# Optimization experiments

Measured on AMD Instinct MI355X. Metric: run time of the kernel, lower is better.

Reference implementation:

```python
import jax, jax.numpy as jnp
import numpy as np

EPS = 1e-5
NH, NP = 4, 4  # num_heads, num_points (num_levels = 1)


def layer_norm(x, g, b):
    m = jnp.mean(x, -1, keepdims=True)
    xc = x - m
    v = jnp.mean(xc * xc, -1, keepdims=True)
    return xc * jax.lax.rsqrt(v + EPS) * g + b


def setup_inputs() -> dict:
    key = jax.random.key(0)
    ks = jax.random.split(key, 8)
    B, C, H, W = 8, 256, 64, 64
    s = 0.02
    return {
        "x1": jax.random.normal(ks[0], (B, C, H, W), jnp.float32),
        "x2": jax.random.normal(ks[1], (B, C, H, W), jnp.float32),
        "ln1_g": jnp.ones((C,), jnp.float32),
        "ln1_b": jnp.zeros((C,), jnp.float32),
        "ln2_g": jnp.ones((C,), jnp.float32),
        "ln2_b": jnp.zeros((C,), jnp.float32),
        "pos_scale": jnp.ones((1,), jnp.float32),
        "W_off": jax.random.normal(ks[2], (C, NH * NP * 2), jnp.float32) * s,
        "b_off": jax.random.normal(ks[3], (NH * NP * 2,), jnp.float32) * 0.5,
        "W_att": jax.random.normal(ks[4], (C, NH * NP), jnp.float32) * s,
        "b_att": jnp.zeros((NH * NP,), jnp.float32),
        "W_val": jax.random.normal(ks[5], (C, C), jnp.float32) * s,
        "b_val": jnp.zeros((C,), jnp.float32),
        "W_out": jax.random.normal(ks[6], (C, C), jnp.float32) * s,
        "b_out": jnp.zeros((C,), jnp.float32),
    }


def reference(x1, x2, ln1_g, ln1_b, ln2_g, ln2_b, pos_scale,
              W_off, b_off, W_att, b_att, W_val, b_val, W_out, b_out):
    B, C, H, W = x1.shape
    Nq = H * W
    d = C // NH
    q_in = x1.reshape(B, C, Nq).transpose(0, 2, 1)   # (B, Nq, C)
    v_in = x2.reshape(B, C, Nq).transpose(0, 2, 1)   # (B, Nv, C), identity

    # ScaledSinuEmbedding positional encoding over the query sequence
    inv_freq = 1.0 / (10000.0 ** (jnp.arange(0, C, 2, dtype=jnp.float32) / C))
    sinu = jnp.arange(Nq, dtype=jnp.float32)[:, None] * inv_freq[None, :]
    qpos = jnp.concatenate([jnp.sin(sinu), jnp.cos(sinu)], -1) * pos_scale  # (Nq, C)

    query = layer_norm(q_in, ln1_g, ln1_b) + qpos[None]
    value = layer_norm(v_in, ln2_g, ln2_b) @ W_val + b_val                 # (B, Nv, C)
    value = value.reshape(B, Nq, NH, d).transpose(0, 2, 1, 3)              # (B, NH, Nv, d)

    off = (query @ W_off + b_off).reshape(B, Nq, NH, NP, 2)
    att = jax.nn.softmax((query @ W_att + b_att).reshape(B, Nq, NH, NP), axis=-1)

    # reference points: normalized pixel centers of the query grid
    ry, rx = jnp.meshgrid((jnp.arange(H, dtype=jnp.float32) + 0.5) / H,
                          (jnp.arange(W, dtype=jnp.float32) + 0.5) / W,
                          indexing="ij")
    ref = jnp.stack([rx.ravel(), ry.ravel()], -1)                          # (Nq, 2) as (x, y)

    norm = jnp.array([W, H], jnp.float32)  # offset_normalizer = (W, H)
    loc = ref[None, :, None, None, :] + off / norm                         # (B,Nq,NH,NP,2)
    loc = loc.transpose(0, 2, 1, 3, 4)                                     # (B,NH,Nq,NP,2)
    # grid_sample(align_corners=False): pixel = normalized * size - 0.5
    px = loc[..., 0] * W - 0.5
    py = loc[..., 1] * H - 0.5
    x0 = jnp.floor(px); y0 = jnp.floor(py)
    wx = px - x0; wy = py - y0
    x0i = x0.astype(jnp.int32); y0i = y0.astype(jnp.int32)

    def gather(ix, iy):
        # zero padding for out-of-bounds corners, like grid_sample(padding_mode='zeros')
        valid = ((ix >= 0) & (ix < W) & (iy >= 0) & (iy < H)).astype(value.dtype)
        idx = jnp.clip(iy, 0, H - 1) * W + jnp.clip(ix, 0, W - 1)          # (B,NH,Nq,NP)
        g = jnp.take_along_axis(value, idx.reshape(B, NH, Nq * NP, 1), axis=2)
        return g.reshape(B, NH, Nq, NP, d) * valid[..., None]

    sampled = (gather(x0i, y0i) * ((1 - wx) * (1 - wy))[..., None]
               + gather(x0i + 1, y0i) * (wx * (1 - wy))[..., None]
               + gather(x0i, y0i + 1) * ((1 - wx) * wy)[..., None]
               + gather(x0i + 1, y0i + 1) * (wx * wy)[..., None])          # (B,NH,Nq,NP,d)

    out = jnp.sum(sampled * att.transpose(0, 2, 1, 3)[..., None], axis=3)  # (B,NH,Nq,d)
    out = out.transpose(0, 2, 1, 3).reshape(B, Nq, C)
    out = out @ W_out + b_out + v_in                                       # + identity (x2)
    return out.transpose(0, 2, 1).reshape(B, C, H, W)
```

## Files before the change

### kernel.cpp

```cpp
#include <hip/hip_runtime.h>
#include <math.h>

namespace {
constexpr int kC = 256;
constexpr int kNq = 4096;
constexpr int kM = 32768;
}

typedef __attribute__((ext_vector_type(8))) short short8;
typedef __attribute__((ext_vector_type(4))) float f32x4;

__device__ inline unsigned short f2bf(float f) {
  union { float f; unsigned u; } v; v.f = f;
  unsigned r = (v.u + 0x7FFFu + ((v.u >> 16) & 1u)) >> 16;
  return (unsigned short)r;
}
__device__ inline float uasf(unsigned u) {
  union { unsigned u; float f; } v; v.u = u; return v.f;
}

__global__ __launch_bounds__(256)
void prep_weights_kernel(const float* __restrict__ Wv, const float* __restrict__ Wo,
                         const float* __restrict__ Woff, const float* __restrict__ Watt,
                         unsigned short* __restrict__ WvT, unsigned short* __restrict__ WoT,
                         unsigned short* __restrict__ WoaT) {
  const int i = blockIdx.x * 256 + threadIdx.x;
  {
    const int n = i >> 8, k = i & 255;
    WvT[i] = f2bf(Wv[k * 256 + n]);
    WoT[i] = f2bf(Wo[k * 256 + n]);
  }
  if (i < 16384) {
    const int j = i >> 8, k = i & 255;
    float v = 0.f;
    if (j < 32) v = Woff[k * 32 + j];
    else if (j < 48) v = Watt[k * 16 + (j - 32)];
    WoaT[i] = f2bf(v);
  }
}

__global__ __launch_bounds__(256)
void fused_ln_gemm_kernel(const float* __restrict__ x1, const float* __restrict__ x2,
                          const float* __restrict__ ln1_g, const float* __restrict__ ln1_b,
                          const float* __restrict__ ln2_g, const float* __restrict__ ln2_b,
                          const float* __restrict__ ps,
                          const unsigned short* __restrict__ WvT,
                          const float* __restrict__ b_val, unsigned short* __restrict__ V,
                          const unsigned short* __restrict__ WoaT,
                          const float* __restrict__ boff, const float* __restrict__ batt,
                          float* __restrict__ RAW) {
  __shared__ unsigned short As[64][264];
  __shared__ float scratch[256][33];
  __shared__ float psum[8][32];
  __shared__ float psq[8][32];
  __shared__ float smean[64];
  __shared__ float srstd[64];

  const int mode = blockIdx.x & 1;
  const int m0 = (blockIdx.x >> 1) * 64;
  const int b = m0 >> 12;
  const int n0 = m0 & 4095;
  const int tid = threadIdx.x;
  const float* X = mode ? x1 : x2;
  const float gc = mode ? ln1_g[tid] : ln2_g[tid];
  const float bc = mode ? ln1_b[tid] : ln2_b[tid];
  float scale = 0.f, invf = 0.f;
  if (mode) {
    scale = ps[0];
    const int i2 = (tid < 128) ? tid : (tid - 128);
    invf = powf(10000.f, -(float)(2 * i2) * (1.f / 256.f));
  }
  const float* Xb = X + (size_t)b * kC * kNq;

  for (int grp = 0; grp < 2; ++grp) {
    float4 vbuf[8];
#pragma unroll
    for (int it = 0; it < 8; ++it) {
      const int i = it * 256 + tid;
      const int c = i >> 3, q4 = (i & 7) * 4;
      vbuf[it] = *(const float4*)&Xb[(size_t)c * kNq + n0 + grp * 32 + q4];
    }
#pragma unroll
    for (int it = 0; it < 8; ++it) {
      const int i = it * 256 + tid;
      const int c = i >> 3, q4 = (i & 7) * 4;
      scratch[c][q4 + 0] = vbuf[it].x;
      scratch[c][q4 + 1] = vbuf[it].y;
      scratch[c][q4 + 2] = vbuf[it].z;
      scratch[c][q4 + 3] = vbuf[it].w;
    }
    __syncthreads();
    {
      const int nn = tid & 31, cg = tid >> 5;
      float s = 0.f, sq = 0.f;
#pragma unroll
      for (int cc = 0; cc < 32; ++cc) {
        const float v = scratch[cg * 32 + cc][nn];
        s += v; sq += v * v;
      }
      psum[cg][nn] = s; psq[cg][nn] = sq;
    }
    __syncthreads();
    if (tid < 32) {
      float S = 0.f, Q = 0.f;
#pragma unroll
      for (int g = 0; g < 8; ++g) { S += psum[g][tid]; Q += psq[g][tid]; }
      const float m = S * (1.f / 256.f);
      const float v = Q * (1.f / 256.f) - m * m;
      smean[grp * 32 + tid] = m;
      srstd[grp * 32 + tid] = rsqrtf(v + 1e-5f);
    }
    __syncthreads();
    if (mode) {
      for (int q = 0; q < 32; ++q) {
        const int row = grp * 32 + q;
        float val = (scratch[tid][q] - smean[row]) * srstd[row] * gc + bc;
        const float a = (float)(n0 + row) * invf;
        val += ((tid < 128) ? sinf(a) : cosf(a)) * scale;
        As[row][tid] = f2bf(val);
      }
    } else {
      for (int q = 0; q < 32; ++q) {
        const int row = grp * 32 + q;
        As[row][tid] = f2bf((scratch[tid][q] - smean[row]) * srstd[row] * gc + bc);
      }
    }
    __syncthreads();
  }

  const int lane = tid & 63, w = tid >> 6;
  const int l15 = lane & 15, quad = lane >> 4;

  if (mode == 0) {
    f32x4 acc[4][4];
#pragma unroll
    for (int i = 0; i < 4; ++i)
#pragma unroll
      for (int j = 0; j < 4; ++j) acc[i][j] = (f32x4){0.f, 0.f, 0.f, 0.f};
#pragma unroll
    for (int s = 0; s < 8; ++s) {
      short8 af[4], wf[4];
#pragma unroll
      for (int t = 0; t < 4; ++t) af[t] = *(const short8*)&As[t * 16 + l15][s * 32 + quad * 8];
#pragma unroll
      for (int t = 0; t < 4; ++t)
        wf[t] = *(const short8*)&WvT[(size_t)(w * 64 + t * 16 + l15) * 256 + s * 32 + quad * 8];
#pragma unroll
      for (int i = 0; i < 4; ++i)
#pragma unroll
        for (int j = 0; j < 4; ++j)
          acc[i][j] = __builtin_amdgcn_mfma_f32_16x16x32_bf16(af[i], wf[j], acc[i][j], 0, 0, 0);
    }
#pragma unroll
    for (int i = 0; i < 4; ++i)
#pragma unroll
      for (int j = 0; j < 4; ++j) {
        const int n = w * 64 + j * 16 + l15;
        const float bn = b_val[n];
#pragma unroll
        for (int r = 0; r < 4; ++r) {
          const int m = m0 + i * 16 + quad * 4 + r;
          V[(size_t)m * 256 + n] = f2bf(acc[i][j][r] + bn);
        }
      }
  } else {
    f32x4 acc[3];
#pragma unroll
    for (int j = 0; j < 3; ++j) acc[j] = (f32x4){0.f, 0.f, 0.f, 0.f};
#pragma unroll
    for (int s = 0; s < 8; ++s) {
      short8 af = *(const short8*)&As[w * 16 + l15][s * 32 + quad * 8];
      short8 wf[3];
#pragma unroll
      for (int t = 0; t < 3; ++t)
        wf[t] = *(const short8*)&WoaT[(size_t)(t * 16 + l15) * 256 + s * 32 + quad * 8];
#pragma unroll
      for (int j = 0; j < 3; ++j)
        acc[j] = __builtin_amdgcn_mfma_f32_16x16x32_bf16(af, wf[j], acc[j], 0, 0, 0);
    }
#pragma unroll
    for (int j = 0; j < 3; ++j) {
      const int n = j * 16 + l15;
      const float bn = (n < 32) ? boff[n] : batt[n - 32];
#pragma unroll
      for (int r = 0; r < 4; ++r) {
        const int m = m0 + w * 16 + quad * 4 + r;
        RAW[(size_t)m * 48 + n] = acc[j][r] + bn;
      }
    }
  }
}

__global__ __launch_bounds__(256)
void sample_out_kernel(const float* __restrict__ RAW, const unsigned short* __restrict__ V,
                       const unsigned short* __restrict__ Wt,
                       const float* __restrict__ bias, const float* __restrict__ x2,
                       float* __restrict__ OUT) {
  __shared__ unsigned short Bs[64][264];
  __shared__ __align__(16) char smemA[32768];
  int (*sidx)[4] = (int(*)[4])smemA;
  float (*swgt)[4] = (float(*)[4])(smemA + 16384);
  float* ot = (float*)smemA;

  const int blk = blockIdx.x;
  const int b = blk & 7;
  const int tile = blk >> 3;
  const int m0 = b * 4096 + tile * 64;
  const int tid = threadIdx.x;

#pragma unroll
  for (int t = 0; t < 4; ++t) {
    const int trip = t * 256 + tid;
    const int q_l = trip >> 4, h = (trip >> 2) & 3, p = trip & 3;
    const int m = m0 + q_l;
    const float* raw = RAW + (size_t)m * 48;
    const float l0 = raw[32 + h * 4 + 0];
    const float l1 = raw[32 + h * 4 + 1];
    const float l2 = raw[32 + h * 4 + 2];
    const float l3 = raw[32 + h * 4 + 3];
    const float mx = fmaxf(fmaxf(l0, l1), fmaxf(l2, l3));
    const float e0 = expf(l0 - mx), e1 = expf(l1 - mx), e2 = expf(l2 - mx), e3 = expf(l3 - mx);
    const float lp = (p == 0) ? e0 : (p == 1) ? e1 : (p == 2) ? e2 : e3;
    const float attp = lp / (e0 + e1 + e2 + e3);

    const float ox = raw[h * 8 + p * 2 + 0];
    const float oy = raw[h * 8 + p * 2 + 1];
    const float px = (float)(m & 63) + ox;
    const float py = (float)((m >> 6) & 63) + oy;
    const float fx = floorf(px), fy = floorf(py);
    const float wx = px - fx, wy = py - fy;
    const int x0 = (int)fx, y0 = (int)fy;
#pragma unroll
    for (int c = 0; c < 4; ++c) {
      const int dx = c & 1, dy = c >> 1;
      const int xx = x0 + dx, yy = y0 + dy;
      const bool valid = (xx >= 0) & (xx < 64) & (yy >= 0) & (yy < 64);
      const float wc = (dx ? wx : 1.f - wx) * (dy ? wy : 1.f - wy) * attp;
      swgt[trip][c] = valid ? wc : 0.f;
      const int xc = min(max(xx, 0), 63), yc = min(max(yy, 0), 63);
      sidx[trip][c] = yc * 64 + xc;
    }
  }
  __syncthreads();

#pragma unroll
  for (int it = 0; it < 8; ++it) {
    const int lin = it * 256 + tid;
    const int q_l = lin >> 5, sub = lin & 31;
    const int h = sub >> 3, c8 = (sub & 7) * 8;
    const int trip0 = q_l * 16 + h * 4;
    const unsigned short* vb = V + (size_t)b * kNq * kC + h * 64 + c8;
    float acc[8] = {};
#pragma unroll
    for (int p = 0; p < 4; ++p) {
      const int4 idx = *(const int4*)&sidx[trip0 + p][0];
      const float4 wv = *(const float4*)&swgt[trip0 + p][0];
      const int ia[4] = {idx.x, idx.y, idx.z, idx.w};
      const float wa[4] = {wv.x, wv.y, wv.z, wv.w};
#pragma unroll
      for (int c = 0; c < 4; ++c) {
        const uint4 u = *(const uint4*)&vb[(size_t)ia[c] * kC];
        const float w = wa[c];
        acc[0] = fmaf(w, uasf(u.x << 16), acc[0]);
        acc[1] = fmaf(w, uasf(u.x & 0xffff0000u), acc[1]);
        acc[2] = fmaf(w, uasf(u.y << 16), acc[2]);
        acc[3] = fmaf(w, uasf(u.y & 0xffff0000u), acc[3]);
        acc[4] = fmaf(w, uasf(u.z << 16), acc[4]);
        acc[5] = fmaf(w, uasf(u.z & 0xffff0000u), acc[5]);
        acc[6] = fmaf(w, uasf(u.w << 16), acc[6]);
        acc[7] = fmaf(w, uasf(u.w & 0xffff0000u), acc[7]);
      }
    }
    short8 outv;
#pragma unroll
    for (int e = 0; e < 8; ++e) outv[e] = (short)f2bf(acc[e]);
    *(short8*)&Bs[q_l][h * 64 + c8] = outv;
  }
  __syncthreads();

  const int lane = tid & 63, w = tid >> 6;
  const int l15 = lane & 15, quad = lane >> 4;
  f32x4 acc[4][4];
#pragma unroll
  for (int i = 0; i < 4; ++i)
#pragma unroll
    for (int j = 0; j < 4; ++j) acc[i][j] = (f32x4){0.f, 0.f, 0.f, 0.f};
#pragma unroll
  for (int s = 0; s < 8; ++s) {
    short8 wf[4], bf[4];
#pragma unroll
    for (int t = 0; t < 4; ++t)
      wf[t] = *(const short8*)&Wt[(size_t)(w * 64 + t * 16 + l15) * 256 + s * 32 + quad * 8];
#pragma unroll
    for (int t = 0; t < 4; ++t) bf[t] = *(const short8*)&Bs[t * 16 + l15][s * 32 + quad * 8];
#pragma unroll
    for (int i = 0; i < 4; ++i)
#pragma unroll
      for (int j = 0; j < 4; ++j)
        acc[i][j] = __builtin_amdgcn_mfma_f32_16x16x32_bf16(wf[i], bf[j], acc[i][j], 0, 0, 0);
  }

  const int whalf = w >> 1;
  const int clbase = (w & 1) * 64;
  for (int ch = 0; ch < 2; ++ch) {
    __syncthreads();
    if (whalf == ch) {
#pragma unroll
      for (int i = 0; i < 4; ++i)
#pragma unroll
        for (int j = 0; j < 4; ++j)
#pragma unroll
          for (int r = 0; r < 4; ++r)
            ot[(clbase + i * 16 + quad * 4 + r) * 64 + j * 16 + l15] = acc[i][j][r];
    }
    __syncthreads();
#pragma unroll
    for (int t = 0; t < 8; ++t) {
      const int lin = t * 256 + tid;
      const int cl = lin >> 4, q4 = (lin & 15) * 4;
      const int c = ch * 128 + cl;
      const size_t rowbase = ((size_t)b * 256 + c) * 4096 + tile * 64;
      const float4 xv = *(const float4*)&x2[rowbase + q4];
      const float bc = bias[c];
      float4 o;
      o.x = ot[cl * 64 + q4 + 0] + bc + xv.x;
      o.y = ot[cl * 64 + q4 + 1] + bc + xv.y;
      o.z = ot[cl * 64 + q4 + 2] + bc + xv.z;
      o.w = ot[cl * 64 + q4 + 3] + bc + xv.w;
      *(float4*)&OUT[rowbase + q4] = o;
    }
  }
}

extern "C" void kernel_launch(void* const* d_in, const int* in_sizes, int n_in,
                              void* d_out, int out_size, void* d_ws, size_t ws_size,
                              hipStream_t stream) {
  const float* x1 = (const float*)d_in[0];
  const float* x2 = (const float*)d_in[1];
  const float* ln1_g = (const float*)d_in[2];
  const float* ln1_b = (const float*)d_in[3];
  const float* ln2_g = (const float*)d_in[4];
  const float* ln2_b = (const float*)d_in[5];
  const float* pos_scale = (const float*)d_in[6];
  const float* W_off = (const float*)d_in[7];
  const float* b_off = (const float*)d_in[8];
  const float* W_att = (const float*)d_in[9];
  const float* b_att = (const float*)d_in[10];
  const float* W_val = (const float*)d_in[11];
  const float* b_val = (const float*)d_in[12];
  const float* W_out = (const float*)d_in[13];
  const float* b_out = (const float*)d_in[14];
  float* out = (float*)d_out;

  char* ws = (char*)d_ws;
  const size_t plane2 = (size_t)kM * kC * sizeof(unsigned short);
  unsigned short* Vb   = (unsigned short*)(ws);
  float* RAW           = (float*)(ws + plane2);
  unsigned short* WvT  = (unsigned short*)(ws + plane2 + (size_t)kM * 48 * 4);
  unsigned short* WoT  = WvT + 65536;
  unsigned short* WoaT = WoT + 65536;

  prep_weights_kernel<<<256, 256, 0, stream>>>(W_val, W_out, W_off, W_att, WvT, WoT, WoaT);
  fused_ln_gemm_kernel<<<1024, 256, 0, stream>>>(x1, x2, ln1_g, ln1_b, ln2_g, ln2_b,
                                                 pos_scale, WvT, b_val, Vb,
                                                 WoaT, b_off, b_att, RAW);
  sample_out_kernel<<<512, 256, 0, stream>>>(RAW, Vb, WoT, b_out, x2, out);
}
```

Before: 185.0 us.

## Precompute positional-encoding projection once; restructure LN stats with register loads and shuffles

Uses linearity to split the offset/attention projection: the positional-encoding term times W_off/W_att plus bias is computed once per query position in the weight-prep kernel (QP) and added in the epilogue. This removes per-element sin/cos from the per-batch LN kernel. The LayerNorm path now loads all input tiles into registers up front, reduces sums with wave shuffles, and stages x in LDS as bf16 instead of fp32. That shrinks LDS use but normalizes from bf16-rounded inputs, which adds precision error.

```diff
diff --git a/kernel.cpp b/kernel.cpp
--- a/kernel.cpp
+++ b/kernel.cpp
@@ -8,6 +8,7 @@
 }
 
 typedef __attribute__((ext_vector_type(8))) short short8;
+typedef __attribute__((ext_vector_type(4))) short short4v;
 typedef __attribute__((ext_vector_type(4))) float f32x4;
 
 __device__ inline unsigned short f2bf(float f) {
@@ -15,6 +16,9 @@
   unsigned r = (v.u + 0x7FFFu + ((v.u >> 16) & 1u)) >> 16;
   return (unsigned short)r;
 }
+__device__ inline float bf2f(unsigned short h) {
+  union { unsigned u; float f; } v; v.u = ((unsigned)h) << 16; return v.f;
+}
 __device__ inline float uasf(unsigned u) {
   union { unsigned u; float f; } v; v.u = u; return v.f;
 }
@@ -22,9 +26,14 @@
 __global__ __launch_bounds__(256)
 void prep_weights_kernel(const float* __restrict__ Wv, const float* __restrict__ Wo,
                          const float* __restrict__ Woff, const float* __restrict__ Watt,
+                         const float* __restrict__ boff, const float* __restrict__ batt,
+                         const float* __restrict__ ps,
                          unsigned short* __restrict__ WvT, unsigned short* __restrict__ WoT,
-                         unsigned short* __restrict__ WoaT) {
-  const int i = blockIdx.x * 256 + threadIdx.x;
+                         unsigned short* __restrict__ WoaT, float* __restrict__ QP) {
+  __shared__ unsigned short Aq[64][264];
+  const int blk = blockIdx.x;
+  const int tid = threadIdx.x;
+  const int i = blk * 256 + tid;
   {
     const int n = i >> 8, k = i & 255;
     WvT[i] = f2bf(Wv[k * 256 + n]);
@@ -37,22 +46,61 @@
     else if (j < 48) v = Watt[k * 16 + (j - 32)];
     WoaT[i] = f2bf(v);
   }
+  if (blk >= 64) return;
+
+  const float scale = ps[0];
+  const int i2 = (tid < 128) ? tid : (tid - 128);
+  const float invf = powf(10000.f, -(float)(2 * i2) * (1.f / 256.f));
+  for (int q = 0; q < 64; ++q) {
+    const float a = (float)(blk * 64 + q) * invf;
+    Aq[q][tid] = f2bf(((tid < 128) ? sinf(a) : cosf(a)) * scale);
+  }
+  __syncthreads();
+
+  const int lane = tid & 63, w = tid >> 6;
+  const int l15 = lane & 15, quad = lane >> 4;
+  f32x4 acc[3];
+#pragma unroll
+  for (int j = 0; j < 3; ++j) acc[j] = (f32x4){0.f, 0.f, 0.f, 0.f};
+#pragma unroll
+  for (int s = 0; s < 8; ++s) {
+    short8 af = *(const short8*)&Aq[w * 16 + l15][s * 32 + quad * 8];
+    short8 wf[3];
+#pragma unroll
+    for (int t = 0; t < 3; ++t)
+#pragma unroll
+      for (int j = 0; j < 8; ++j) {
+        const int k = s * 32 + quad * 8 + j;
+        wf[t][j] = (short)f2bf((t < 2) ? Woff[k * 32 + t * 16 + l15]
+                                       : Watt[k * 16 + l15]);
+      }
+#pragma unroll
+    for (int j = 0; j < 3; ++j)
+      acc[j] = __builtin_amdgcn_mfma_f32_16x16x32_bf16(af, wf[j], acc[j], 0, 0, 0);
+  }
+#pragma unroll
+  for (int j = 0; j < 3; ++j) {
+    const int n = j * 16 + l15;
+    const float bn = (n < 32) ? boff[n] : batt[n - 32];
+#pragma unroll
+    for (int r = 0; r < 4; ++r) {
+      const int q = blk * 64 + w * 16 + quad * 4 + r;
+      QP[q * 48 + n] = acc[j][r] + bn;
+    }
+  }
 }
 
 __global__ __launch_bounds__(256)
 void fused_ln_gemm_kernel(const float* __restrict__ x1, const float* __restrict__ x2,
                           const float* __restrict__ ln1_g, const float* __restrict__ ln1_b,
                           const float* __restrict__ ln2_g, const float* __restrict__ ln2_b,
-                          const float* __restrict__ ps,
                           const unsigned short* __restrict__ WvT,
                           const float* __restrict__ b_val, unsigned short* __restrict__ V,
                           const unsigned short* __restrict__ WoaT,
-                          const float* __restrict__ boff, const float* __restrict__ batt,
-                          float* __restrict__ RAW) {
+                          const float* __restrict__ QP, float* __restrict__ RAW) {
   __shared__ unsigned short As[64][264];
-  __shared__ float scratch[256][33];
-  __shared__ float psum[8][32];
-  __shared__ float psq[8][32];
+  __shared__ unsigned short sx[256][36];
+  __shared__ float psum[2][32][4];
   __shared__ float smean[64];
   __shared__ float srstd[64];
 
@@ -61,74 +109,72 @@
   const int b = m0 >> 12;
   const int n0 = m0 & 4095;
   const int tid = threadIdx.x;
-  const float* X = mode ? x1 : x2;
+  const int lane = tid & 63, w = tid >> 6;
   const float gc = mode ? ln1_g[tid] : ln2_g[tid];
   const float bc = mode ? ln1_b[tid] : ln2_b[tid];
-  float scale = 0.f, invf = 0.f;
-  if (mode) {
-    scale = ps[0];
-    const int i2 = (tid < 128) ? tid : (tid - 128);
-    invf = powf(10000.f, -(float)(2 * i2) * (1.f / 256.f));
-  }
-  const float* Xb = X + (size_t)b * kC * kNq;
-
-  for (int grp = 0; grp < 2; ++grp) {
-    float4 vbuf[8];
+  const float* Xb = (mode ? x1 : x2) + (size_t)b * kC * kNq;
+
+  const int cbase = tid >> 3;
+  const int q4 = (tid & 7) * 4;
+  float4 v[16];
+#pragma unroll
+  for (int g = 0; g < 2; ++g)
+#pragma unroll
+    for (int it = 0; it < 8; ++it)
+      v[g * 8 + it] = *(const float4*)&Xb[(size_t)(it * 32 + cbase) * kNq + n0 + g * 32 + q4];
+
+  for (int g = 0; g < 2; ++g) {
+    float s[4] = {0.f, 0.f, 0.f, 0.f}, sq[4] = {0.f, 0.f, 0.f, 0.f};
 #pragma unroll
     for (int it = 0; it < 8; ++it) {
-      const int i = it * 256 + tid;
-      const int c = i >> 3, q4 = (i & 7) * 4;
-      vbuf[it] = *(const float4*)&Xb[(size_t)c * kNq + n0 + grp * 32 + q4];
-    }
-#pragma unroll
-    for (int it = 0; it < 8; ++it) {
-      const int i = it * 256 + tid;
-      const int c = i >> 3, q4 = (i & 7) * 4;
-      scratch[c][q4 + 0] = vbuf[it].x;
-      scratch[c][q4 + 1] = vbuf[it].y;
-      scratch[c][q4 + 2] = vbuf[it].z;
-      scratch[c][q4 + 3] = vbuf[it].w;
-    }
-    __syncthreads();
-    {
-      const int nn = tid & 31, cg = tid >> 5;
-      float s = 0.f, sq = 0.f;
-#pragma unroll
-      for (int cc = 0; cc < 32; ++cc) {
-        const float v = scratch[cg * 32 + cc][nn];
-        s += v; sq += v * v;
-      }
-      psum[cg][nn] = s; psq[cg][nn] = sq;
+      const float4 f4 = v[g * 8 + it];
+      const float e[4] = {f4.x, f4.y, f4.z, f4.w};
+      short4v pk;
+#pragma unroll
+      for (int j = 0; j < 4; ++j) {
+        s[j] += e[j];
+        sq[j] += e[j] * e[j];
+        pk[j] = (short)f2bf(e[j]);
+      }
+      *(short4v*)&sx[it * 32 + cbase][q4] = pk;
+    }
+#pragma unroll
+    for (int d = 8; d <= 32; d <<= 1)
+#pragma unroll
+      for (int j = 0; j < 4; ++j) {
+        s[j] += __shfl_xor(s[j], d);
+        sq[j] += __shfl_xor(sq[j], d);
+      }
+    if (lane < 8) {
+#pragma unroll
+      for (int j = 0; j < 4; ++j) {
+        psum[0][lane * 4 + j][w] = s[j];
+        psum[1][lane * 4 + j][w] = sq[j];
+      }
     }
     __syncthreads();
     if (tid < 32) {
       float S = 0.f, Q = 0.f;
 #pragma unroll
-      for (int g = 0; g < 8; ++g) { S += psum[g][tid]; Q += psq[g][tid]; }
+      for (int ww = 0; ww < 4; ++ww) { S += psum[0][tid][ww]; Q += psum[1][tid][ww]; }
       const float m = S * (1.f / 256.f);
-      const float v = Q * (1.f / 256.f) - m * m;
-      smean[grp * 32 + tid] = m;
-      srstd[grp * 32 + tid] = rsqrtf(v + 1e-5f);
+      const float var = Q * (1.f / 256.f) - m * m;
+      smean[g * 32 + tid] = m;
+      srstd[g * 32 + tid] = rsqrtf(var + 1e-5f);
     }
     __syncthreads();
-    if (mode) {
-      for (int q = 0; q < 32; ++q) {
-        const int row = grp * 32 + q;
-        float val = (scratch[tid][q] - smean[row]) * srstd[row] * gc + bc;
-        const float a = (float)(n0 + row) * invf;
-        val += ((tid < 128) ? sinf(a) : cosf(a)) * scale;
-        As[row][tid] = f2bf(val);
-      }
-    } else {
-      for (int q = 0; q < 32; ++q) {
-        const int row = grp * 32 + q;
-        As[row][tid] = f2bf((scratch[tid][q] - smean[row]) * srstd[row] * gc + bc);
+#pragma unroll
+    for (int k = 0; k < 8; ++k) {
+      const short4v xs = *(const short4v*)&sx[tid][k * 4];
+#pragma unroll
+      for (int j = 0; j < 4; ++j) {
+        const int row = g * 32 + k * 4 + j;
+        As[row][tid] = f2bf((bf2f((unsigned short)xs[j]) - smean[row]) * srstd[row] * gc + bc);
       }
     }
     __syncthreads();
   }
 
-  const int lane = tid & 63, w = tid >> 6;
   const int l15 = lane & 15, quad = lane >> 4;
 
   if (mode == 0) {
@@ -181,11 +227,11 @@
 #pragma unroll
     for (int j = 0; j < 3; ++j) {
       const int n = j * 16 + l15;
-      const float bn = (n < 32) ? boff[n] : batt[n - 32];
 #pragma unroll
       for (int r = 0; r < 4; ++r) {
         const int m = m0 + w * 16 + quad * 4 + r;
-        RAW[(size_t)m * 48 + n] = acc[j][r] + bn;
+        const int q = n0 + w * 16 + quad * 4 + r;
+        RAW[(size_t)m * 48 + n] = acc[j][r] + QP[q * 48 + n];
       }
     }
   }
@@ -359,10 +405,12 @@
   unsigned short* WvT  = (unsigned short*)(ws + plane2 + (size_t)kM * 48 * 4);
   unsigned short* WoT  = WvT + 65536;
   unsigned short* WoaT = WoT + 65536;
-
-  prep_weights_kernel<<<256, 256, 0, stream>>>(W_val, W_out, W_off, W_att, WvT, WoT, WoaT);
+  float* QP            = (float*)(WoaT + 16384);
+
+  prep_weights_kernel<<<256, 256, 0, stream>>>(W_val, W_out, W_off, W_att,
+                                               b_off, b_att, pos_scale,
+                                               WvT, WoT, WoaT, QP);
   fused_ln_gemm_kernel<<<1024, 256, 0, stream>>>(x1, x2, ln1_g, ln1_b, ln2_g, ln2_b,
-                                                 pos_scale, WvT, b_val, Vb,
-                                                 WoaT, b_off, b_att, RAW);
+                                                 WvT, b_val, Vb, WoaT, QP, RAW);
   sample_out_kernel<<<512, 256, 0, stream>>>(RAW, Vb, WoT, b_out, x2, out);
 }
```

Result: slower. 192.5 us (+4.0%).
